# Performance work log

Hardware: AMD Instinct MI355X
Metric: run time of the kernel (lower is better)

## Reference

```python
import jax, jax.numpy as jnp
import numpy as np

B, N, M = 1, 3000, 3000        # surface points, query points
K = N + M                       # nodes per graph
IN, HID, H, OUT = 3, 64, 4, 2   # in_channels, hidden_channels, heads, out_channels
RADIUS2 = 0.05 ** 2
NEG_SLOPE = 0.2
NEG_INF = jnp.float32(-1e9)


def setup_inputs() -> dict:
    key = jax.random.key(0)
    ks = jax.random.split(key, 12)
    s1 = 1.0 / np.sqrt(IN)
    s2 = 1.0 / np.sqrt(H * HID)
    return {
        "pos": jax.random.uniform(ks[0], (B, 3, N), dtype=jnp.float32),
        "pos_non_manifold": jax.random.uniform(ks[1], (B, 3, M), dtype=jnp.float32),
        # GAT layer 1: lin weight, attention vectors (per head), bias
        "W1": jax.random.normal(ks[2], (IN, H * HID), dtype=jnp.float32) * s1,
        "a_src1": jax.random.normal(ks[3], (H, HID), dtype=jnp.float32) * s2,
        "a_dst1": jax.random.normal(ks[4], (H, HID), dtype=jnp.float32) * s2,
        "b1": jnp.zeros((H * HID,), dtype=jnp.float32),
        # GAT layer 2
        "W2": jax.random.normal(ks[5], (H * HID, H * HID), dtype=jnp.float32) * s2,
        "a_src2": jax.random.normal(ks[6], (H, HID), dtype=jnp.float32) * s2,
        "a_dst2": jax.random.normal(ks[7], (H, HID), dtype=jnp.float32) * s2,
        "b2": jnp.zeros((H * HID,), dtype=jnp.float32),
        # final fc
        "fc_w": jax.random.normal(ks[8], (H * HID, OUT), dtype=jnp.float32) * s2,
        "fc_b": jnp.zeros((OUT,), dtype=jnp.float32),
    }


def _gat_layer(x, mask, W, a_src, a_dst, b):
    # x: [B,K,Fin]; mask: [B,K,K] (mask[b,i,j] True if edge j->i, symmetric, incl. diag)
    h = (x @ W).reshape(x.shape[0], x.shape[1], H, HID)        # [B,K,H,C]
    es = jnp.einsum('bjhc,hc->bjh', h, a_src)                   # source score
    ed = jnp.einsum('bihc,hc->bih', h, a_dst)                   # destination score
    e = ed[:, :, None, :] + es[:, None, :, :]                   # [B,i,j,H]
    e = jnp.where(e >= 0, e, NEG_SLOPE * e)                     # LeakyReLU(0.2)
    e = jnp.where(mask[..., None], e, NEG_INF)
    alpha = jax.nn.softmax(e, axis=2)                           # softmax over sources j
    out = jnp.einsum('bijh,bjhc->bihc', alpha, h)               # [B,K,H,C]
    return out.reshape(x.shape[0], x.shape[1], H * HID) + b


def reference(pos, pos_non_manifold, W1, a_src1, a_dst1, b1,
              W2, a_src2, a_dst2, b2, fc_w, fc_b):
    # cat along point dim then transpose -> [B, K, 3]
    pts = jnp.concatenate([pos, pos_non_manifold], axis=2).transpose(0, 2, 1)
    # squared cdist via gram trick (avoids [B,K,K,3] intermediate)
    sq = jnp.sum(pts * pts, axis=-1)                            # [B,K]
    d2 = sq[:, :, None] + sq[:, None, :] - 2.0 * jnp.einsum('bid,bjd->bij', pts, pts)
    mask = d2 < RADIUS2                                         # adjacency (block-diag per batch)
    x = jax.nn.relu(_gat_layer(pts, mask, W1, a_src1, a_dst1, b1))
    x = jax.nn.relu(_gat_layer(x, mask, W2, a_src2, a_dst2, b2))
    x = x @ fc_w + fc_b                                         # [B,K,OUT]
    # original: x[:, num_points:].reshape(B, OUT, 3000) with num_points = M
    logits = x[:, M:].reshape(pts.shape[0], OUT, 3000)
    return logits
```

## Files before the change

kernel.cpp:

```cpp
#include <hip/hip_runtime.h>

#define NPTS   3000
#define MPTS   3000
#define KNODES 6000
#define HEADS  4
#define FDIM   256
#define OUTC   2
#define R2     0.0025f
#define NSLOPE 0.2f
#define MAXNBR 64
#define RPB    8

#define OFF_ES2  0
#define OFF_ED2  24000
#define OFF_X    48000
#define OFF_H2   1584000
#define OFF_END  3120000

__device__ __forceinline__ float wsum(float v) {
#pragma unroll
    for (int off = 32; off; off >>= 1) v += __shfl_xor(v, off, 64);
    return v;
}

__global__ __launch_bounds__(256) void k_nbrx(
        const float* __restrict__ pos, const float* __restrict__ pnm,
        const float* __restrict__ W1, const float* __restrict__ as1,
        const float* __restrict__ ad1, const float* __restrict__ b1,
        float* __restrict__ x, int* __restrict__ cnt, int* __restrict__ idx) {
    __shared__ int   s_cnt[RPB];
    __shared__ int   s_idx[RPB][MAXNBR];
    __shared__ float s_u[HEADS][3], s_v[HEADS][3];
    __shared__ float s_q[RPB][HEADS][3];
    const int t = threadIdx.x;
    const int i0 = blockIdx.x * RPB;
    if (t < RPB) s_cnt[t] = 0;

    const float w1a = W1[t], w1b = W1[FDIM + t], w1c = W1[2 * FDIM + t];
    {
        const float asv = as1[t], adv = ad1[t];
        float u0 = wsum(w1a * asv), u1 = wsum(w1b * asv), u2 = wsum(w1c * asv);
        float v0 = wsum(w1a * adv), v1 = wsum(w1b * adv), v2 = wsum(w1c * adv);
        if ((t & 63) == 0) {
            int h = t >> 6;
            s_u[h][0] = u0; s_u[h][1] = u1; s_u[h][2] = u2;
            s_v[h][0] = v0; s_v[h][1] = v1; s_v[h][2] = v2;
        }
    }
    __syncthreads();

    const float* base = (i0 < NPTS) ? pos : pnm;
    const int ib = (i0 < NPTS) ? i0 : i0 - NPTS;
    float xi[RPB], yi[RPB], zi[RPB], si[RPB];
#pragma unroll
    for (int r = 0; r < RPB; ++r) {
        float px = base[ib + r], py = base[NPTS + ib + r], pz = base[2 * NPTS + ib + r];
        xi[r] = px; yi[r] = py; zi[r] = pz;
        si[r] = __fadd_rn(__fadd_rn(__fmul_rn(px, px), __fmul_rn(py, py)),
                          __fmul_rn(pz, pz));
    }
    for (int j = t; j < KNODES; j += 256) {
        float xj, yj, zj;
        if (j < NPTS) { xj = pos[j]; yj = pos[NPTS + j]; zj = pos[2 * NPTS + j]; }
        else { int q = j - NPTS; xj = pnm[q]; yj = pnm[MPTS + q]; zj = pnm[2 * MPTS + q]; }
        float sj = __fadd_rn(__fadd_rn(__fmul_rn(xj, xj), __fmul_rn(yj, yj)),
                             __fmul_rn(zj, zj));
#pragma unroll
        for (int r = 0; r < RPB; ++r) {
            float dot = __fadd_rn(__fadd_rn(__fmul_rn(xi[r], xj), __fmul_rn(yi[r], yj)),
                                  __fmul_rn(zi[r], zj));
            float d2 = __fsub_rn(__fadd_rn(si[r], sj), __fmul_rn(2.0f, dot));
            if (d2 < R2) {
                int p = atomicAdd(&s_cnt[r], 1);
                if (p < MAXNBR) s_idx[r][p] = j;
            }
        }
    }
    __syncthreads();
    if (t < RPB) cnt[i0 + t] = min(s_cnt[t], MAXNBR);
#pragma unroll
    for (int r = 0; r < RPB; ++r) {
        int c = min(s_cnt[r], MAXNBR);
        if (t < c) idx[(i0 + r) * MAXNBR + t] = s_idx[r][t];
    }

    {
        const int pr = (t & 31) >> 2, h = t & 3;
        const int c = min(s_cnt[pr], MAXNBR);
        const float u0 = s_u[h][0], u1 = s_u[h][1], u2 = s_u[h][2];
        const float dsum = fmaf(xi[pr], s_v[h][0],
                           fmaf(yi[pr], s_v[h][1], zi[pr] * s_v[h][2]));
        float m = -1e30f;
        for (int jl = 0; jl < c; ++jl) {
            int j = s_idx[pr][jl];
            float xj, yj, zj;
            if (j < NPTS) { xj = pos[j]; yj = pos[NPTS + j]; zj = pos[2 * NPTS + j]; }
            else { int q = j - NPTS; xj = pnm[q]; yj = pnm[MPTS + q]; zj = pnm[2 * MPTS + q]; }
            float e = dsum + fmaf(xj, u0, fmaf(yj, u1, zj * u2));
            e = (e >= 0.f) ? e : NSLOPE * e;
            m = fmaxf(m, e);
        }
        float S = 0.f, q0 = 0.f, q1 = 0.f, q2 = 0.f;
        for (int jl = 0; jl < c; ++jl) {
            int j = s_idx[pr][jl];
            float xj, yj, zj;
            if (j < NPTS) { xj = pos[j]; yj = pos[NPTS + j]; zj = pos[2 * NPTS + j]; }
            else { int q = j - NPTS; xj = pnm[q]; yj = pnm[MPTS + q]; zj = pnm[2 * MPTS + q]; }
            float e = dsum + fmaf(xj, u0, fmaf(yj, u1, zj * u2));
            e = (e >= 0.f) ? e : NSLOPE * e;
            float a = __expf(e - m);
            S += a;
            q0 = fmaf(a, xj, q0); q1 = fmaf(a, yj, q1); q2 = fmaf(a, zj, q2);
        }
        if (t < 32) {
            float inv = 1.f / S;
            s_q[pr][h][0] = q0 * inv;
            s_q[pr][h][1] = q1 * inv;
            s_q[pr][h][2] = q2 * inv;
        }
    }
    __syncthreads();

    {
        const float b1v = b1[t];
        const int h = t >> 6;
#pragma unroll
        for (int r = 0; r < RPB; ++r) {
            float q0 = s_q[r][h][0], q1 = s_q[r][h][1], q2 = s_q[r][h][2];
            float v = fmaf(q0, w1a, fmaf(q1, w1b, q2 * w1c)) + b1v;
            x[(size_t)(i0 + r) * FDIM + t] = fmaxf(v, 0.f);
        }
    }
}

__global__ __launch_bounds__(256) void k_gemm2(
        const float* __restrict__ x, const float* __restrict__ W2,
        const float* __restrict__ as2, const float* __restrict__ ad2,
        float* __restrict__ h2, float* __restrict__ es2, float* __restrict__ ed2) {
    const int t = threadIdx.x;
    const int i0 = __builtin_amdgcn_readfirstlane(blockIdx.x * RPB);
    float acc[RPB];
#pragma unroll
    for (int r = 0; r < RPB; ++r) acc[r] = 0.f;
#pragma unroll 2
    for (int k4 = 0; k4 < FDIM / 4; ++k4) {
        float w0 = W2[(4 * k4 + 0) * FDIM + t];
        float w1 = W2[(4 * k4 + 1) * FDIM + t];
        float w2 = W2[(4 * k4 + 2) * FDIM + t];
        float w3 = W2[(4 * k4 + 3) * FDIM + t];
#pragma unroll
        for (int r = 0; r < RPB; ++r) {
            float4 xv = *(const float4*)(x + (size_t)(i0 + r) * FDIM + 4 * k4);
            acc[r] = fmaf(xv.x, w0, fmaf(xv.y, w1, fmaf(xv.z, w2,
                     fmaf(xv.w, w3, acc[r]))));
        }
    }
#pragma unroll
    for (int r = 0; r < RPB; ++r)
        h2[(size_t)(i0 + r) * FDIM + t] = acc[r];
    const float as2v = as2[t], ad2v = ad2[t];
    const int wv = t >> 6, lane = t & 63;
#pragma unroll
    for (int r = 0; r < RPB; ++r) {
        float s = wsum(acc[r] * as2v);
        float d = wsum(acc[r] * ad2v);
        if (lane == 0) {
            es2[(i0 + r) * HEADS + wv] = s;
            ed2[(i0 + r) * HEADS + wv] = d;
        }
    }
}

__global__ void k_agg2fc(const float* __restrict__ h, const float* __restrict__ es,
                         const float* __restrict__ ed, const int* __restrict__ cnt,
                         const int* __restrict__ idx, const float* __restrict__ bias,
                         const float* __restrict__ fw, const float* __restrict__ fb,
                         float* __restrict__ out) {
    __shared__ int   s_idx[MAXNBR];
    __shared__ float s_e[MAXNBR * HEADS];
    __shared__ float s_ed[HEADS];
    __shared__ float s_red[8];
    int q = blockIdx.x;
    int i = MPTS + q;
    int t = threadIdx.x;
    int c = cnt[i];
    if (t < c) s_idx[t] = idx[i * MAXNBR + t];
    if (t < HEADS) s_ed[t] = ed[i * HEADS + t];
    __syncthreads();
    if (t < c * HEADS) {
        int jl = t >> 2, hh = t & 3;
        float e = s_ed[hh] + es[s_idx[jl] * HEADS + hh];
        e = (e >= 0.f) ? e : NSLOPE * e;
        s_e[jl * HEADS + hh] = e;
    }
    __syncthreads();
    int hh = t >> 6;
    float m = -1e30f;
    for (int jl = 0; jl < c; ++jl) m = fmaxf(m, s_e[jl * HEADS + hh]);
    float ssum = 0.f, acc = 0.f;
    for (int jl = 0; jl < c; ++jl) {
        float p = __expf(s_e[jl * HEADS + hh] - m);
        ssum += p;
        acc = fmaf(p, h[s_idx[jl] * FDIM + t], acc);
    }
    float v = fmaxf(acc / ssum + bias[t], 0.f);
    float p0 = v * fw[t * OUTC + 0];
    float p1 = v * fw[t * OUTC + 1];
    for (int off = 32; off; off >>= 1) {
        p0 += __shfl_down(p0, off, 64);
        p1 += __shfl_down(p1, off, 64);
    }
    if ((t & 63) == 0) {
        s_red[(t >> 6) * 2 + 0] = p0;
        s_red[(t >> 6) * 2 + 1] = p1;
    }
    __syncthreads();
    if (t == 0) {
        out[q * OUTC + 0] = s_red[0] + s_red[2] + s_red[4] + s_red[6] + fb[0];
        out[q * OUTC + 1] = s_red[1] + s_red[3] + s_red[5] + s_red[7] + fb[1];
    }
}

extern "C" void kernel_launch(void* const* d_in, const int* in_sizes, int n_in,
                              void* d_out, int out_size, void* d_ws, size_t ws_size,
                              hipStream_t stream) {
    const float* pos   = (const float*)d_in[0];
    const float* pnm   = (const float*)d_in[1];
    const float* W1    = (const float*)d_in[2];
    const float* asrc1 = (const float*)d_in[3];
    const float* adst1 = (const float*)d_in[4];
    const float* b1    = (const float*)d_in[5];
    const float* W2    = (const float*)d_in[6];
    const float* asrc2 = (const float*)d_in[7];
    const float* adst2 = (const float*)d_in[8];
    const float* b2    = (const float*)d_in[9];
    const float* fcw   = (const float*)d_in[10];
    const float* fcb   = (const float*)d_in[11];
    float* out = (float*)d_out;

    float* w    = (float*)d_ws;
    float* es2  = w + OFF_ES2;
    float* ed2  = w + OFF_ED2;
    float* x    = w + OFF_X;
    float* h2   = w + OFF_H2;
    int* nbr_cnt = (int*)((char*)d_ws + (size_t)4 * OFF_END);
    int* nbr_idx = nbr_cnt + KNODES;

    k_nbrx<<<KNODES / RPB, 256, 0, stream>>>(pos, pnm, W1, asrc1, adst1, b1,
                                             x, nbr_cnt, nbr_idx);
    k_gemm2<<<KNODES / RPB, 256, 0, stream>>>(x, W2, asrc2, adst2, h2, es2, ed2);
    k_agg2fc<<<MPTS, FDIM, 0, stream>>>(h2, es2, ed2, nbr_cnt, nbr_idx, b2,
                                        fcw, fcb, out);
}
```

Measured before the change: 138.8 us.

## Fuse layer-1 aggregation with layer-2 GEMM and cache neighbor coords in LDS

Merges the neighbor/layer-1 kernel with the layer-2 linear kernel. The layer-1 output x is kept in shared memory instead of being written to and re-read from global memory, and one kernel launch is removed. Neighbor coordinates are also stored in LDS when neighbors are found, so the softmax loops no longer gather positions from global memory. The cost is higher LDS use per block, which may lower occupancy.

```diff
diff --git a/kernel.cpp b/kernel.cpp
--- a/kernel.cpp
+++ b/kernel.cpp
@@ -13,9 +13,8 @@
 
 #define OFF_ES2  0
 #define OFF_ED2  24000
-#define OFF_X    48000
-#define OFF_H2   1584000
-#define OFF_END  3120000
+#define OFF_H2   48000
+#define OFF_END  1584000
 
 __device__ __forceinline__ float wsum(float v) {
 #pragma unroll
@@ -23,15 +22,20 @@
     return v;
 }
 
-__global__ __launch_bounds__(256) void k_nbrx(
+__global__ __launch_bounds__(256) void k_main(
         const float* __restrict__ pos, const float* __restrict__ pnm,
         const float* __restrict__ W1, const float* __restrict__ as1,
         const float* __restrict__ ad1, const float* __restrict__ b1,
-        float* __restrict__ x, int* __restrict__ cnt, int* __restrict__ idx) {
+        const float* __restrict__ W2, const float* __restrict__ as2,
+        const float* __restrict__ ad2,
+        float* __restrict__ h2, float* __restrict__ es2, float* __restrict__ ed2,
+        int* __restrict__ cnt, int* __restrict__ idx) {
     __shared__ int   s_cnt[RPB];
     __shared__ int   s_idx[RPB][MAXNBR];
+    __shared__ float s_nx[RPB][MAXNBR], s_ny[RPB][MAXNBR], s_nz[RPB][MAXNBR];
     __shared__ float s_u[HEADS][3], s_v[HEADS][3];
     __shared__ float s_q[RPB][HEADS][3];
+    __shared__ __align__(16) float xs[RPB][FDIM];
     const int t = threadIdx.x;
     const int i0 = blockIdx.x * RPB;
     if (t < RPB) s_cnt[t] = 0;
@@ -72,7 +76,10 @@
             float d2 = __fsub_rn(__fadd_rn(si[r], sj), __fmul_rn(2.0f, dot));
             if (d2 < R2) {
                 int p = atomicAdd(&s_cnt[r], 1);
-                if (p < MAXNBR) s_idx[r][p] = j;
+                if (p < MAXNBR) {
+                    s_idx[r][p] = j;
+                    s_nx[r][p] = xj; s_ny[r][p] = yj; s_nz[r][p] = zj;
+                }
             }
         }
     }
@@ -92,20 +99,14 @@
                            fmaf(yi[pr], s_v[h][1], zi[pr] * s_v[h][2]));
         float m = -1e30f;
         for (int jl = 0; jl < c; ++jl) {
-            int j = s_idx[pr][jl];
-            float xj, yj, zj;
-            if (j < NPTS) { xj = pos[j]; yj = pos[NPTS + j]; zj = pos[2 * NPTS + j]; }
-            else { int q = j - NPTS; xj = pnm[q]; yj = pnm[MPTS + q]; zj = pnm[2 * MPTS + q]; }
-            float e = dsum + fmaf(xj, u0, fmaf(yj, u1, zj * u2));
+            float e = dsum + fmaf(s_nx[pr][jl], u0,
+                             fmaf(s_ny[pr][jl], u1, s_nz[pr][jl] * u2));
             e = (e >= 0.f) ? e : NSLOPE * e;
             m = fmaxf(m, e);
         }
         float S = 0.f, q0 = 0.f, q1 = 0.f, q2 = 0.f;
         for (int jl = 0; jl < c; ++jl) {
-            int j = s_idx[pr][jl];
-            float xj, yj, zj;
-            if (j < NPTS) { xj = pos[j]; yj = pos[NPTS + j]; zj = pos[2 * NPTS + j]; }
-            else { int q = j - NPTS; xj = pnm[q]; yj = pnm[MPTS + q]; zj = pnm[2 * MPTS + q]; }
+            float xj = s_nx[pr][jl], yj = s_ny[pr][jl], zj = s_nz[pr][jl];
             float e = dsum + fmaf(xj, u0, fmaf(yj, u1, zj * u2));
             e = (e >= 0.f) ? e : NSLOPE * e;
             float a = __expf(e - m);
@@ -128,45 +129,40 @@
         for (int r = 0; r < RPB; ++r) {
             float q0 = s_q[r][h][0], q1 = s_q[r][h][1], q2 = s_q[r][h][2];
             float v = fmaf(q0, w1a, fmaf(q1, w1b, q2 * w1c)) + b1v;
-            x[(size_t)(i0 + r) * FDIM + t] = fmaxf(v, 0.f);
-        }
-    }
-}
-
-__global__ __launch_bounds__(256) void k_gemm2(
-        const float* __restrict__ x, const float* __restrict__ W2,
-        const float* __restrict__ as2, const float* __restrict__ ad2,
-        float* __restrict__ h2, float* __restrict__ es2, float* __restrict__ ed2) {
-    const int t = threadIdx.x;
-    const int i0 = __builtin_amdgcn_readfirstlane(blockIdx.x * RPB);
-    float acc[RPB];
-#pragma unroll
-    for (int r = 0; r < RPB; ++r) acc[r] = 0.f;
+            xs[r][t] = fmaxf(v, 0.f);
+        }
+    }
+    __syncthreads();
+    {
+        float acc[RPB];
+#pragma unroll
+        for (int r = 0; r < RPB; ++r) acc[r] = 0.f;
 #pragma unroll 2
-    for (int k4 = 0; k4 < FDIM / 4; ++k4) {
-        float w0 = W2[(4 * k4 + 0) * FDIM + t];
-        float w1 = W2[(4 * k4 + 1) * FDIM + t];
-        float w2 = W2[(4 * k4 + 2) * FDIM + t];
-        float w3 = W2[(4 * k4 + 3) * FDIM + t];
+        for (int k4 = 0; k4 < FDIM / 4; ++k4) {
+            float w0 = W2[(4 * k4 + 0) * FDIM + t];
+            float w1 = W2[(4 * k4 + 1) * FDIM + t];
+            float w2 = W2[(4 * k4 + 2) * FDIM + t];
+            float w3 = W2[(4 * k4 + 3) * FDIM + t];
+#pragma unroll
+            for (int r = 0; r < RPB; ++r) {
+                float4 xv = ((const float4*)xs[r])[k4];
+                acc[r] = fmaf(xv.x, w0, fmaf(xv.y, w1, fmaf(xv.z, w2,
+                         fmaf(xv.w, w3, acc[r]))));
+            }
+        }
+#pragma unroll
+        for (int r = 0; r < RPB; ++r)
+            h2[(size_t)(i0 + r) * FDIM + t] = acc[r];
+        const float as2v = as2[t], ad2v = ad2[t];
+        const int wv = t >> 6, lane = t & 63;
 #pragma unroll
         for (int r = 0; r < RPB; ++r) {
-            float4 xv = *(const float4*)(x + (size_t)(i0 + r) * FDIM + 4 * k4);
-            acc[r] = fmaf(xv.x, w0, fmaf(xv.y, w1, fmaf(xv.z, w2,
-                     fmaf(xv.w, w3, acc[r]))));
-        }
-    }
-#pragma unroll
-    for (int r = 0; r < RPB; ++r)
-        h2[(size_t)(i0 + r) * FDIM + t] = acc[r];
-    const float as2v = as2[t], ad2v = ad2[t];
-    const int wv = t >> 6, lane = t & 63;
-#pragma unroll
-    for (int r = 0; r < RPB; ++r) {
-        float s = wsum(acc[r] * as2v);
-        float d = wsum(acc[r] * ad2v);
-        if (lane == 0) {
-            es2[(i0 + r) * HEADS + wv] = s;
-            ed2[(i0 + r) * HEADS + wv] = d;
+            float s = wsum(acc[r] * as2v);
+            float d = wsum(acc[r] * ad2v);
+            if (lane == 0) {
+                es2[(i0 + r) * HEADS + wv] = s;
+                ed2[(i0 + r) * HEADS + wv] = d;
+            }
         }
     }
 }
@@ -241,14 +237,13 @@
     float* w    = (float*)d_ws;
     float* es2  = w + OFF_ES2;
     float* ed2  = w + OFF_ED2;
-    float* x    = w + OFF_X;
     float* h2   = w + OFF_H2;
     int* nbr_cnt = (int*)((char*)d_ws + (size_t)4 * OFF_END);
     int* nbr_idx = nbr_cnt + KNODES;
 
-    k_nbrx<<<KNODES / RPB, 256, 0, stream>>>(pos, pnm, W1, asrc1, adst1, b1,
-                                             x, nbr_cnt, nbr_idx);
-    k_gemm2<<<KNODES / RPB, 256, 0, stream>>>(x, W2, asrc2, adst2, h2, es2, ed2);
+    k_main<<<KNODES / RPB, 256, 0, stream>>>(pos, pnm, W1, asrc1, adst1, b1,
+                                             W2, asrc2, adst2, h2, es2, ed2,
+                                             nbr_cnt, nbr_idx);
     k_agg2fc<<<MPTS, FDIM, 0, stream>>>(h2, es2, ed2, nbr_cnt, nbr_idx, b2,
                                         fcw, fcb, out);
 }
```

Result: faster. 128.9 us (-7.1%).
